# Optimization experiments

Measured on AMD Instinct MI355X. Metric: run time of the kernel, lower is better.

Reference implementation:

```python
import jax, jax.numpy as jnp
import numpy as np

N, K, D, VOCAB = 20000, 32, 128, 100000
NEG = -1e30  # finite large-negative so all-masked rows don't produce NaN softmax


def setup_inputs() -> dict:
    key = jax.random.key(0)
    ks = jax.random.split(key, 10)
    return {
        "nodes": jax.random.randint(ks[0], (N,), 0, VOCAB),
        "neigh_idx": jax.random.randint(ks[1], (N, K), 0, VOCAB),
        "neigh_len": jax.random.randint(ks[2], (N,), 0, K + 1),
        "u2e": jax.random.normal(ks[3], (VOCAB, D), dtype=jnp.float32),
        "W1": jax.random.normal(ks[4], (D, 2 * D), dtype=jnp.float32) * 0.05,
        "b1": jax.random.normal(ks[5], (D,), dtype=jnp.float32) * 0.05,
        "W2": jax.random.normal(ks[6], (D, D), dtype=jnp.float32) * 0.05,
        "b2": jax.random.normal(ks[7], (D,), dtype=jnp.float32) * 0.05,
        "W3": jax.random.normal(ks[8], (1, D), dtype=jnp.float32) * 0.05,
        "b3": jax.random.normal(ks[9], (1,), dtype=jnp.float32) * 0.05,
    }


def reference(nodes, neigh_idx, neigh_len, u2e, W1, b1, W2, b2, W3, b3):
    # self features: [N, D]
    self_feats = u2e[nodes]
    # neighbor features gather: [N, K, D]
    e_u = u2e[neigh_idx]
    # GraphRec Attention: cat(neighbor, self-broadcast) -> MLP -> softmax over K
    x = jnp.concatenate(
        [e_u, jnp.broadcast_to(self_feats[:, None, :], e_u.shape)], axis=-1
    )  # [N, K, 2D]
    h = jax.nn.relu(jnp.einsum("nkf,df->nkd", x, W1) + b1)
    h = jax.nn.relu(jnp.einsum("nkd,ed->nke", h, W2) + b2)
    logits = jnp.einsum("nkd,od->nko", h, W3)[..., 0] + b3[0]  # [N, K]
    mask = jnp.arange(K)[None, :] < neigh_len[:, None]  # [N, K]
    att = jax.nn.softmax(jnp.where(mask, logits, NEG), axis=1)
    att = jnp.where(mask, att, 0.0)  # zero out padded slots (and all-empty rows)
    # attention-weighted neighbor aggregation: [N, D]
    agg = jnp.einsum("nk,nkd->nd", att, e_u)
    has_neigh = (neigh_len > 0)[:, None]
    return jnp.where(has_neigh, (agg + self_feats) * 0.5, self_feats)
```

## Files before the change

### kernel.cpp

```cpp
#include <hip/hip_runtime.h>
#include <hip/hip_bf16.h>
#include <stdint.h>

#define KN 32
#define D  128
#define NNODES 20000
#define GRID 2500
#define ITERS 4
#define VOCAB 100000

#define CONV_BLOCKS 6250
#define PACK_BLOCKS 192
#define SV1_BLOCKS  ((NNODES + 63) / 64)
#define AUX_BLOCKS  (CONV_BLOCKS + PACK_BLOCKS + SV1_BLOCKS)

typedef __bf16 bf16;
typedef __bf16 bf16x8 __attribute__((ext_vector_type(8)));
typedef float  f32x4  __attribute__((ext_vector_type(4)));

#define CHUNK_E 520
#define EU_NODE_E (8 * CHUNK_E)
#define H_STRIDE 136
#define CHUNK_DW 260

#define GL2LDS(src, dst) __builtin_amdgcn_global_load_lds(                 \
    (const __attribute__((address_space(1))) void*)(src),                  \
    (__attribute__((address_space(3))) void*)(dst), 16, 0, 0)

#define MFMA(a, b, c) __builtin_amdgcn_mfma_f32_16x16x32_bf16((a), (b), (c), 0, 0, 0)

__global__ __launch_bounds__(256) void aux_kernel(
    const float* __restrict__ u2e,
    const float* __restrict__ W1,
    const float* __restrict__ W2,
    const int*   __restrict__ nodes,
    bf16*  __restrict__ u2e_bf,
    bf16*  __restrict__ w1p,
    bf16*  __restrict__ w2p,
    float* __restrict__ sv1t)
{
    const int b = blockIdx.x;
    const int t = threadIdx.x;

    if (b < CONV_BLOCKS) {
        size_t i = ((size_t)b * 256 + t) * 8;
        float4 a = *(const float4*)(u2e + i);
        float4 c = *(const float4*)(u2e + i + 4);
        bf16x8 v;
        v[0]=(bf16)a.x; v[1]=(bf16)a.y; v[2]=(bf16)a.z; v[3]=(bf16)a.w;
        v[4]=(bf16)c.x; v[5]=(bf16)c.y; v[6]=(bf16)c.z; v[7]=(bf16)c.w;
        *(bf16x8*)(u2e_bf + i) = v;
        return;
    }
    if (b < CONV_BLOCKS + PACK_BLOCKS) {
        int g = (b - CONV_BLOCKS) * 256 + t;
        if (g < 32768) {
            int j = g & 7, lane = (g >> 3) & 63, kt = (g >> 9) & 7, nt = g >> 12;
            int d = nt * 16 + (lane & 15);
            int f = kt * 32 + ((lane >> 4) << 3) + j;
            w1p[g] = (bf16)W1[d * 256 + f];
        } else if (g < 49152) {
            int u = g - 32768;
            int j = u & 7, lane = (u >> 3) & 63, kt = (u >> 9) & 3, nt = u >> 11;
            int e  = nt * 16 + (lane & 15);
            int dd = kt * 32 + ((lane >> 4) << 3) + j;
            w2p[u] = (bf16)W2[e * 128 + dd];
        }
        return;
    }
    {
        __shared__ alignas(16) float sr[2 * 16 * CHUNK_DW];

        const int sb   = b - CONV_BLOCKS - PACK_BLOCKS;
        const int base = sb * 64;
        const int lane = t & 63;
        const int wave = t >> 6;
        const int ln15 = lane & 15;
        const int quad = lane >> 4;

        {
            const int grp  = wave & 1;
            const int cb   = (wave >> 1) * 8;
            const int half = lane >> 5;
            const int colb = (lane & 31) << 4;
            #pragma unroll
            for (int j = 0; j < 8; ++j) {
                int chunk = cb + j;
                int row = base + grp * 32 + chunk + half * 16;
                int node = nodes[row < NNODES ? row : NNODES - 1];
                GL2LDS((const char*)(u2e + (size_t)node * D) + colb,
                       sr + grp * 16 * CHUNK_DW + chunk * CHUNK_DW);
            }
        }
        __syncthreads();

        const float* g  = sr + (wave & 1) * 16 * CHUNK_DW;
        const int    r0 = ln15 * CHUNK_DW;

        #pragma unroll 1
        for (int np = (wave >> 1) * 2; np <= (wave >> 1) * 2 + 1; ++np) {
            const int nt0 = np * 2;
            bf16x8 b0[4], b1[4];
            #pragma unroll
            for (int kt = 0; kt < 4; ++kt) {
                const float* s0 = W1 + (size_t)(nt0 * 16 + ln15) * 256 + 128 + kt * 32 + quad * 8;
                const float* s1 = W1 + (size_t)((nt0 + 1) * 16 + ln15) * 256 + 128 + kt * 32 + quad * 8;
                f32x4 u0 = *(const f32x4*)(s0), u1 = *(const f32x4*)(s0 + 4);
                f32x4 v0 = *(const f32x4*)(s1), v1 = *(const f32x4*)(s1 + 4);
                bf16x8 bb0, bb1;
                #pragma unroll
                for (int e = 0; e < 4; ++e) {
                    bb0[e] = (bf16)u0[e]; bb0[4 + e] = (bf16)u1[e];
                    bb1[e] = (bf16)v0[e]; bb1[4 + e] = (bf16)v1[e];
                }
                b0[kt] = bb0; b1[kt] = bb1;
            }
            f32x4 c00 = {0.f,0.f,0.f,0.f}, c01 = c00, c10 = c00, c11 = c00;
            #pragma unroll
            for (int kt = 0; kt < 4; ++kt) {
                int off = kt * 32 + quad * 8;
                f32x4 u0 = *(const f32x4*)(g + r0 + off);
                f32x4 u1 = *(const f32x4*)(g + r0 + off + 4);
                f32x4 v0 = *(const f32x4*)(g + r0 + 128 + off);
                f32x4 v1 = *(const f32x4*)(g + r0 + 128 + off + 4);
                bf16x8 a0, a1;
                #pragma unroll
                for (int e = 0; e < 4; ++e) {
                    a0[e] = (bf16)u0[e]; a0[4 + e] = (bf16)u1[e];
                    a1[e] = (bf16)v0[e]; a1[4 + e] = (bf16)v1[e];
                }
                c00 = MFMA(a0, b0[kt], c00);
                c01 = MFMA(a0, b1[kt], c01);
                c10 = MFMA(a1, b0[kt], c10);
                c11 = MFMA(a1, b1[kt], c11);
            }
            #pragma unroll
            for (int r = 0; r < 4; ++r) {
                int row = quad * 4 + r;
                int gr0 = base + (wave & 1) * 32 + row;
                int gr1 = gr0 + 16;
                if (gr0 < NNODES) {
                    sv1t[(size_t)gr0 * D + nt0 * 16 + ln15]       = c00[r];
                    sv1t[(size_t)gr0 * D + (nt0 + 1) * 16 + ln15] = c01[r];
                }
                if (gr1 < NNODES) {
                    sv1t[(size_t)gr1 * D + nt0 * 16 + ln15]       = c10[r];
                    sv1t[(size_t)gr1 * D + (nt0 + 1) * 16 + ln15] = c11[r];
                }
            }
        }
    }
}

__global__ __launch_bounds__(256, 4) void graphrec_agg_kernel(
    const int*   __restrict__ nodes,
    const int*   __restrict__ neigh_idx,
    const int*   __restrict__ neigh_len,
    const float* __restrict__ u2e,
    const bf16*  __restrict__ u2e_bf,
    const float* __restrict__ sv1t,
    const float* __restrict__ b1,
    const float* __restrict__ b2,
    const float* __restrict__ W3,
    const float* __restrict__ b3,
    const bf16*  __restrict__ w1p,
    const bf16*  __restrict__ w2p,
    float*       __restrict__ out)
{
    __shared__ alignas(16) bf16  eu[2 * EU_NODE_E];
    __shared__ alignas(16) float self_f[2 * D];
    __shared__ alignas(16) bf16  h1[2 * KN * H_STRIDE];
    __shared__ float lpart[2][4 * KN];

    const int t    = threadIdx.x;
    const int lane = t & 63;
    const int wave = t >> 6;
    const int ln15 = lane & 15;
    const int quad = lane >> 4;
    const int nt0  = wave * 2;

    const float bias1_0 = b1[nt0 * 16 + ln15];
    const float bias1_1 = b1[(nt0 + 1) * 16 + ln15];
    const float bias2_0 = b2[nt0 * 16 + ln15];
    const float bias2_1 = b2[(nt0 + 1) * 16 + ln15];
    const float w3_0    = W3[nt0 * 16 + ln15];
    const float w3_1    = W3[(nt0 + 1) * 16 + ln15];
    const float b3v     = b3[0];

    bf16x8 w1r[2][4];
    #pragma unroll
    for (int nt = 0; nt < 2; ++nt)
        #pragma unroll
        for (int ft = 0; ft < 4; ++ft)
            w1r[nt][ft] = *(const bf16x8*)(w1p + ((nt0 + nt) * 8 + ft) * 512 + lane * 8);
    bf16x8 w2r[2][4];
    #pragma unroll
    for (int nt = 0; nt < 2; ++nt)
        #pragma unroll
        for (int kt = 0; kt < 4; ++kt)
            w2r[nt][kt] = *(const bf16x8*)(w2p + ((nt0 + nt) * 4 + kt) * 512 + lane * 8);

    #pragma unroll 1
    for (int it = 0; it < ITERS; ++it) {
        const int nA   = blockIdx.x * 8 + it * 2;
        const int lenA = neigh_len[nA];
        const int lenB = neigh_len[nA + 1];

        const float svA0 = sv1t[(size_t)nA * D + nt0 * 16 + ln15];
        const float svA1 = sv1t[(size_t)nA * D + (nt0 + 1) * 16 + ln15];
        const float svB0 = sv1t[(size_t)(nA + 1) * D + nt0 * 16 + ln15];
        const float svB1 = sv1t[(size_t)(nA + 1) * D + (nt0 + 1) * 16 + ln15];

        {
            const int gnd = wave >> 1;
            const int cb  = (wave & 1) * 4;
            #pragma unroll
            for (int j = 0; j < 4; ++j) {
                int chunk = cb + j;
                int idx = neigh_idx[(nA + gnd) * KN + chunk + ((lane >> 4) << 3)];
                GL2LDS(u2e_bf + (size_t)idx * D + ((lane & 15) << 3),
                       eu + gnd * EU_NODE_E + chunk * CHUNK_E);
            }
            if (wave == 0) {
                int sidx = nodes[nA + (lane >> 5)];
                GL2LDS(u2e + (size_t)sidx * D + ((lane & 31) << 2), self_f);
            }
        }
        __syncthreads();

        #pragma unroll 1
        for (int nd = 0; nd < 2; ++nd) {
            const bf16* euN = eu + nd * EU_NODE_E;
            bf16* h1N = h1 + nd * KN * H_STRIDE;

            f32x4 c00 = {0.f,0.f,0.f,0.f}, c01 = c00, c10 = c00, c11 = c00;
            const int rb = (ln15 & 7) * CHUNK_E + (ln15 >> 3) * 128;
            #pragma unroll
            for (int ft = 0; ft < 4; ++ft) {
                bf16x8 a0 = *(const bf16x8*)(euN + rb + ft * 32 + quad * 8);
                bf16x8 a1 = *(const bf16x8*)(euN + rb + 256 + ft * 32 + quad * 8);
                c00 = MFMA(a0, w1r[0][ft], c00);
                c01 = MFMA(a0, w1r[1][ft], c01);
                c10 = MFMA(a1, w1r[0][ft], c10);
                c11 = MFMA(a1, w1r[1][ft], c11);
            }
            const float s0 = nd ? svB0 : svA0;
            const float s1 = nd ? svB1 : svA1;
            #pragma unroll
            for (int r = 0; r < 4; ++r) {
                int row = quad * 4 + r;
                h1N[row * H_STRIDE + nt0 * 16 + ln15]              = (bf16)fmaxf(c00[r] + bias1_0 + s0, 0.f);
                h1N[row * H_STRIDE + (nt0 + 1) * 16 + ln15]        = (bf16)fmaxf(c01[r] + bias1_1 + s1, 0.f);
                h1N[(16 + row) * H_STRIDE + nt0 * 16 + ln15]       = (bf16)fmaxf(c10[r] + bias1_0 + s0, 0.f);
                h1N[(16 + row) * H_STRIDE + (nt0 + 1) * 16 + ln15] = (bf16)fmaxf(c11[r] + bias1_1 + s1, 0.f);
            }
        }
        __syncthreads();

        #pragma unroll 1
        for (int nd = 0; nd < 2; ++nd) {
            const bf16* h1N = h1 + nd * KN * H_STRIDE;
            f32x4 d00 = {0.f,0.f,0.f,0.f}, d01 = d00, d10 = d00, d11 = d00;
            #pragma unroll
            for (int kt = 0; kt < 4; ++kt) {
                bf16x8 a0 = *(const bf16x8*)(h1N + ln15 * H_STRIDE + kt * 32 + quad * 8);
                bf16x8 a1 = *(const bf16x8*)(h1N + (16 + ln15) * H_STRIDE + kt * 32 + quad * 8);
                d00 = MFMA(a0, w2r[0][kt], d00);
                d01 = MFMA(a0, w2r[1][kt], d01);
                d10 = MFMA(a1, w2r[0][kt], d10);
                d11 = MFMA(a1, w2r[1][kt], d11);
            }
            #pragma unroll
            for (int r = 0; r < 4; ++r) {
                float p0 = w3_0 * fmaxf(d00[r] + bias2_0, 0.f)
                         + w3_1 * fmaxf(d01[r] + bias2_1, 0.f);
                float p1 = w3_0 * fmaxf(d10[r] + bias2_0, 0.f)
                         + w3_1 * fmaxf(d11[r] + bias2_1, 0.f);
                #pragma unroll
                for (int o = 1; o < 16; o <<= 1) {
                    p0 += __shfl_xor(p0, o);
                    p1 += __shfl_xor(p1, o);
                }
                if (ln15 == 0) {
                    lpart[nd][wave * KN + quad * 4 + r]      = p0;
                    lpart[nd][wave * KN + 16 + quad * 4 + r] = p1;
                }
            }
        }
        __syncthreads();

        {
            const int nd    = wave >> 1;
            const int dbase = (wave & 1) * 64;
            const int g     = lane >> 3;
            const int l3    = lane & 7;
            const int k     = lane & 31;

            float lg = lpart[nd][k] + lpart[nd][KN + k] + lpart[nd][2 * KN + k]
                     + lpart[nd][3 * KN + k] + b3v;
            const int len = nd ? lenB : lenA;
            bool act = k < len;
            float l = act ? lg : -1e30f;
            float m = l;
            #pragma unroll
            for (int o = 1; o < 32; o <<= 1) m = fmaxf(m, __shfl_xor(m, o));
            float e = act ? expf(l - m) : 0.f;
            float s = e;
            #pragma unroll
            for (int o = 1; o < 32; o <<= 1) s += __shfl_xor(s, o);
            float att = (s > 0.f) ? (e / s) : 0.f;

            const bf16* euN = eu + nd * EU_NODE_E;
            float acc[8] = {0.f,0.f,0.f,0.f,0.f,0.f,0.f,0.f};
            #pragma unroll
            for (int p = 0; p < 4; ++p) {
                int kk = p * 8 + g;
                float attk = __shfl(att, kk);
                bf16x8 v = *(const bf16x8*)(euN + g * CHUNK_E + p * 128 + dbase + l3 * 8);
                #pragma unroll
                for (int j = 0; j < 8; ++j) acc[j] += attk * (float)v[j];
            }
            #pragma unroll
            for (int j = 0; j < 8; ++j) {
                acc[j] += __shfl_xor(acc[j], 8);
                acc[j] += __shfl_xor(acc[j], 16);
                acc[j] += __shfl_xor(acc[j], 32);
            }
            if (g == 0) {
                const float* sfp = self_f + nd * D + dbase + l3 * 8;
                f32x4 sf0 = *(const f32x4*)(sfp);
                f32x4 sf1 = *(const f32x4*)(sfp + 4);
                f32x4 o0, o1;
                #pragma unroll
                for (int j = 0; j < 4; ++j) {
                    o0[j] = (len > 0) ? 0.5f * (acc[j] + sf0[j])     : sf0[j];
                    o1[j] = (len > 0) ? 0.5f * (acc[4 + j] + sf1[j]) : sf1[j];
                }
                float* op = out + (size_t)(nA + nd) * D + dbase + l3 * 8;
                *(f32x4*)(op)     = o0;
                *(f32x4*)(op + 4) = o1;
            }
        }
        __syncthreads();
    }
}

#define FB_EU_NODE_DW (16 * CHUNK_DW)

__global__ __launch_bounds__(256) void pack_weights_kernel(
    const float* __restrict__ W1, const float* __restrict__ W2,
    bf16* __restrict__ w1p, bf16* __restrict__ w2p)
{
    int t = blockIdx.x * 256 + threadIdx.x;
    if (t < 32768) {
        int j = t & 7, lane = (t >> 3) & 63, kt = (t >> 9) & 7, nt = t >> 12;
        int d = nt * 16 + (lane & 15);
        int f = kt * 32 + ((lane >> 4) << 3) + j;
        w1p[t] = (bf16)W1[d * 256 + f];
    } else if (t < 49152) {
        int u = t - 32768;
        int j = u & 7, lane = (u >> 3) & 63, kt = (u >> 9) & 3, nt = u >> 11;
        int e  = nt * 16 + (lane & 15);
        int dd = kt * 32 + ((lane >> 4) << 3) + j;
        w2p[u] = (bf16)W2[e * 128 + dd];
    }
}

__global__ __launch_bounds__(256, 3) void graphrec_agg_fb(
    const int*   __restrict__ nodes,
    const int*   __restrict__ neigh_idx,
    const int*   __restrict__ neigh_len,
    const float* __restrict__ u2e,
    const float* __restrict__ b1,
    const float* __restrict__ b2,
    const float* __restrict__ W3,
    const float* __restrict__ b3,
    const bf16*  __restrict__ w1p,
    const bf16*  __restrict__ w2p,
    float*       __restrict__ out)
{
    __shared__ alignas(16) float eu[2 * FB_EU_NODE_DW];
    __shared__ alignas(16) bf16  h1[2 * KN * H_STRIDE];
    __shared__ alignas(16) float self_f[2 * D];
    __shared__ float lpart[2][4 * KN];
    __shared__ float att_s[2][KN];

    const int t    = threadIdx.x;
    const int lane = t & 63;
    const int wave = t >> 6;
    const int ln15 = lane & 15;
    const int quad = lane >> 4;
    const int nt0  = wave * 2;

    const float bias1_0 = b1[nt0 * 16 + ln15];
    const float bias1_1 = b1[(nt0 + 1) * 16 + ln15];
    const float bias2_0 = b2[nt0 * 16 + ln15];
    const float bias2_1 = b2[(nt0 + 1) * 16 + ln15];
    const float w3_0    = W3[nt0 * 16 + ln15];
    const float w3_1    = W3[(nt0 + 1) * 16 + ln15];
    const float b3v     = b3[0];

    bf16x8 w1r[2][8];
    #pragma unroll
    for (int nt = 0; nt < 2; ++nt)
        #pragma unroll
        for (int ft = 0; ft < 8; ++ft)
            w1r[nt][ft] = *(const bf16x8*)(w1p + ((nt0 + nt) * 8 + ft) * 512 + lane * 8);
    bf16x8 w2r[2][4];
    #pragma unroll
    for (int nt = 0; nt < 2; ++nt)
        #pragma unroll
        for (int kt = 0; kt < 4; ++kt)
            w2r[nt][kt] = *(const bf16x8*)(w2p + ((nt0 + nt) * 4 + kt) * 512 + lane * 8);

    #pragma unroll 1
    for (int it = 0; it < ITERS; ++it) {
        const int nA   = blockIdx.x * 8 + it * 2;
        const int lenA = neigh_len[nA];
        const int lenB = neigh_len[nA + 1];
        {
            const int half = lane >> 5;
            const int colb = (lane & 31) << 4;
            #pragma unroll
            for (int nd = 0; nd < 2; ++nd) {
                #pragma unroll
                for (int j = 0; j < 4; ++j) {
                    int chunk = wave * 4 + j;
                    int idx = neigh_idx[(nA + nd) * KN + chunk + (half << 4)];
                    const char* src = (const char*)(u2e + (size_t)idx * D) + colb;
                    GL2LDS(src, eu + nd * FB_EU_NODE_DW + chunk * CHUNK_DW);
                }
            }
            if (wave == 0) {
                int sidx = nodes[nA + half];
                const char* src = (const char*)(u2e + (size_t)sidx * D) + colb;
                GL2LDS(src, self_f);
            }
        }
        __syncthreads();
        #pragma unroll 1
        for (int nd = 0; nd < 2; ++nd) {
            const float* euN = eu + nd * FB_EU_NODE_DW;
            const float* sfN = self_f + nd * D;
            bf16* h1N = h1 + nd * KN * H_STRIDE;
            f32x4 c00 = {0.f,0.f,0.f,0.f}, c01 = c00, c10 = c00, c11 = c00;
            const int r0 = ln15 * CHUNK_DW;
            #pragma unroll
            for (int ft = 0; ft < 4; ++ft) {
                int off = ft * 32 + quad * 8;
                f32x4 u0 = *(const f32x4*)(euN + r0 + off);
                f32x4 u1 = *(const f32x4*)(euN + r0 + off + 4);
                f32x4 v0 = *(const f32x4*)(euN + r0 + 128 + off);
                f32x4 v1 = *(const f32x4*)(euN + r0 + 128 + off + 4);
                bf16x8 a0, a1;
                #pragma unroll
                for (int e = 0; e < 4; ++e) {
                    a0[e] = (bf16)u0[e]; a0[4 + e] = (bf16)u1[e];
                    a1[e] = (bf16)v0[e]; a1[4 + e] = (bf16)v1[e];
                }
                c00 = MFMA(a0, w1r[0][ft], c00);
                c01 = MFMA(a0, w1r[1][ft], c01);
                c10 = MFMA(a1, w1r[0][ft], c10);
                c11 = MFMA(a1, w1r[1][ft], c11);
            }
            #pragma unroll
            for (int ft = 4; ft < 8; ++ft) {
                int off = (ft - 4) * 32 + quad * 8;
                f32x4 u0 = *(const f32x4*)(sfN + off);
                f32x4 u1 = *(const f32x4*)(sfN + off + 4);
                bf16x8 a;
                #pragma unroll
                for (int e = 0; e < 4; ++e) { a[e] = (bf16)u0[e]; a[4 + e] = (bf16)u1[e]; }
                c00 = MFMA(a, w1r[0][ft], c00);
                c01 = MFMA(a, w1r[1][ft], c01);
                c10 = MFMA(a, w1r[0][ft], c10);
                c11 = MFMA(a, w1r[1][ft], c11);
            }
            #pragma unroll
            for (int r = 0; r < 4; ++r) {
                int row = quad * 4 + r;
                h1N[row * H_STRIDE + nt0 * 16 + ln15]              = (bf16)fmaxf(c00[r] + bias1_0, 0.f);
                h1N[row * H_STRIDE + (nt0 + 1) * 16 + ln15]        = (bf16)fmaxf(c01[r] + bias1_1, 0.f);
                h1N[(16 + row) * H_STRIDE + nt0 * 16 + ln15]       = (bf16)fmaxf(c10[r] + bias1_0, 0.f);
                h1N[(16 + row) * H_STRIDE + (nt0 + 1) * 16 + ln15] = (bf16)fmaxf(c11[r] + bias1_1, 0.f);
            }
        }
        __syncthreads();
        #pragma unroll 1
        for (int nd = 0; nd < 2; ++nd) {
            const bf16* h1N = h1 + nd * KN * H_STRIDE;
            f32x4 d00 = {0.f,0.f,0.f,0.f}, d01 = d00, d10 = d00, d11 = d00;
            #pragma unroll
            for (int kt = 0; kt < 4; ++kt) {
                bf16x8 a0 = *(const bf16x8*)(h1N + ln15 * H_STRIDE + kt * 32 + quad * 8);
                bf16x8 a1 = *(const bf16x8*)(h1N + (16 + ln15) * H_STRIDE + kt * 32 + quad * 8);
                d00 = MFMA(a0, w2r[0][kt], d00);
                d01 = MFMA(a0, w2r[1][kt], d01);
                d10 = MFMA(a1, w2r[0][kt], d10);
                d11 = MFMA(a1, w2r[1][kt], d11);
            }
            #pragma unroll
            for (int r = 0; r < 4; ++r) {
                float p0 = w3_0 * fmaxf(d00[r] + bias2_0, 0.f)
                         + w3_1 * fmaxf(d01[r] + bias2_1, 0.f);
                float p1 = w3_0 * fmaxf(d10[r] + bias2_0, 0.f)
                         + w3_1 * fmaxf(d11[r] + bias2_1, 0.f);
                #pragma unroll
                for (int o = 1; o < 16; o <<= 1) {
                    p0 += __shfl_xor(p0, o);
                    p1 += __shfl_xor(p1, o);
                }
                if (ln15 == 0) {
                    lpart[nd][wave * KN + quad * 4 + r]      = p0;
                    lpart[nd][wave * KN + 16 + quad * 4 + r] = p1;
                }
            }
        }
        __syncthreads();
        if (wave < 2) {
            int nd = wave, k = lane & 31;
            float lg = lpart[nd][k] + lpart[nd][KN + k] + lpart[nd][2 * KN + k]
                     + lpart[nd][3 * KN + k] + b3v;
            int len = nd ? lenB : lenA;
            bool act = (lane < 32) && (k < len);
            float l = act ? lg : -1e30f;
            float m = l;
            #pragma unroll
            for (int o = 1; o < 32; o <<= 1) m = fmaxf(m, __shfl_xor(m, o));
            float e = act ? expf(l - m) : 0.f;
            float s = e;
            #pragma unroll
            for (int o = 1; o < 32; o <<= 1) s += __shfl_xor(s, o);
            if (lane < 32) att_s[nd][k] = (s > 0.f) ? (e / s) : 0.f;
        }
        __syncthreads();
        {
            int nd = t >> 7, d = t & 127;
            const float* euN = eu + nd * FB_EU_NODE_DW;
            float acc = 0.f;
            #pragma unroll
            for (int k = 0; k < KN; ++k)
                acc += att_s[nd][k] * euN[(k & 15) * CHUNK_DW + ((k >> 4) << 7) + d];
            float sf = self_f[nd * D + d];
            int len = nd ? lenB : lenA;
            out[(size_t)(nA + nd) * D + d] = (len > 0) ? 0.5f * (acc + sf) : sf;
        }
        __syncthreads();
    }
}

extern "C" void kernel_launch(void* const* d_in, const int* in_sizes, int n_in,
                              void* d_out, int out_size, void* d_ws, size_t ws_size,
                              hipStream_t stream) {
    const int*   nodes     = (const int*)d_in[0];
    const int*   neigh_idx = (const int*)d_in[1];
    const int*   neigh_len = (const int*)d_in[2];
    const float* u2e       = (const float*)d_in[3];
    const float* W1        = (const float*)d_in[4];
    const float* b1        = (const float*)d_in[5];
    const float* W2        = (const float*)d_in[6];
    const float* b2        = (const float*)d_in[7];
    const float* W3        = (const float*)d_in[8];
    const float* b3        = (const float*)d_in[9];
    float* out = (float*)d_out;

    bf16*  w1p    = (bf16*)d_ws;
    bf16*  w2p    = w1p + 32768;
    bf16*  u2e_bf = (bf16*)((char*)d_ws + 98304);
    float* sv1t   = (float*)((char*)d_ws + 98304 + (size_t)VOCAB * D * 2);
    const size_t need = 98304ull + (size_t)VOCAB * D * 2 + (size_t)NNODES * D * 4;

    if (ws_size >= need) {
        aux_kernel<<<AUX_BLOCKS, 256, 0, stream>>>(u2e, W1, W2, nodes,
                                                   u2e_bf, w1p, w2p, sv1t);
        graphrec_agg_kernel<<<GRID, 256, 0, stream>>>(nodes, neigh_idx, neigh_len,
                                                      u2e, u2e_bf, sv1t, b1, b2,
                                                      W3, b3, w1p, w2p, out);
    } else {
        pack_weights_kernel<<<192, 256, 0, stream>>>(W1, W2, w1p, w2p);
        graphrec_agg_fb<<<GRID, 256, 0, stream>>>(nodes, neigh_idx, neigh_len, u2e,
                                                  b1, b2, W3, b3, w1p, w2p, out);
    }
}
```

Before: 223.1 us.

## Double-buffer neighbor gathers into LDS and simplify per-lane aggregation

Gathered neighbor and self rows now go into two alternating LDS buffers. Each iteration issues the global-to-LDS loads for the next node pair before computing the current one, so the random-access gather overlaps with the MFMA work. Barriers that only guard LDS traffic become a cheaper lgkmcnt wait plus s_barrier. The trailing sync is dropped. The weighted aggregation now has each lane own one feature column and loop over all 32 neighbors with shuffles and scalar LDS reads, replacing the vectorized partial sums and cross-lane reduction. The doubled LDS footprint lowers the occupancy hint from 4 to 3 blocks, and the new aggregation issues many more shuffles and scalar LDS loads.

```diff
diff --git a/kernel.cpp b/kernel.cpp
--- a/kernel.cpp
+++ b/kernel.cpp
@@ -28,6 +28,12 @@
     (__attribute__((address_space(3))) void*)(dst), 16, 0, 0)
 
 #define MFMA(a, b, c) __builtin_amdgcn_mfma_f32_16x16x32_bf16((a), (b), (c), 0, 0, 0)
+
+__device__ __forceinline__ void bar_lds() {
+    asm volatile("s_waitcnt lgkmcnt(0)" ::: "memory");
+    __builtin_amdgcn_s_barrier();
+    asm volatile("" ::: "memory");
+}
 
 __global__ __launch_bounds__(256) void aux_kernel(
     const float* __restrict__ u2e,
@@ -152,7 +158,7 @@
     }
 }
 
-__global__ __launch_bounds__(256, 4) void graphrec_agg_kernel(
+__global__ __launch_bounds__(256, 3) void graphrec_agg_kernel(
     const int*   __restrict__ nodes,
     const int*   __restrict__ neigh_idx,
     const int*   __restrict__ neigh_len,
@@ -167,8 +173,8 @@
     const bf16*  __restrict__ w2p,
     float*       __restrict__ out)
 {
-    __shared__ alignas(16) bf16  eu[2 * EU_NODE_E];
-    __shared__ alignas(16) float self_f[2 * D];
+    __shared__ alignas(16) bf16  eu[2][2 * EU_NODE_E];
+    __shared__ alignas(16) float self_f[2][2 * D];
     __shared__ alignas(16) bf16  h1[2 * KN * H_STRIDE];
     __shared__ float lpart[2][4 * KN];
 
@@ -200,8 +206,27 @@
         for (int kt = 0; kt < 4; ++kt)
             w2r[nt][kt] = *(const bf16x8*)(w2p + ((nt0 + nt) * 4 + kt) * 512 + lane * 8);
 
+    const int gnd = wave >> 1;
+    const int cb  = (wave & 1) * 4;
+
+    {
+        const int nA0 = blockIdx.x * 8;
+        #pragma unroll
+        for (int j = 0; j < 4; ++j) {
+            int chunk = cb + j;
+            int idx = neigh_idx[(nA0 + gnd) * KN + chunk + ((lane >> 4) << 3)];
+            GL2LDS(u2e_bf + (size_t)idx * D + ((lane & 15) << 3),
+                   &eu[0][gnd * EU_NODE_E + chunk * CHUNK_E]);
+        }
+        if (wave == 0) {
+            int sidx = nodes[nA0 + (lane >> 5)];
+            GL2LDS(u2e + (size_t)sidx * D + ((lane & 31) << 2), &self_f[0][0]);
+        }
+    }
+
     #pragma unroll 1
     for (int it = 0; it < ITERS; ++it) {
+        const int buf  = it & 1;
         const int nA   = blockIdx.x * 8 + it * 2;
         const int lenA = neigh_len[nA];
         const int lenB = neigh_len[nA + 1];
@@ -211,26 +236,26 @@
         const float svB0 = sv1t[(size_t)(nA + 1) * D + nt0 * 16 + ln15];
         const float svB1 = sv1t[(size_t)(nA + 1) * D + (nt0 + 1) * 16 + ln15];
 
-        {
-            const int gnd = wave >> 1;
-            const int cb  = (wave & 1) * 4;
+        __syncthreads();
+
+        if (it + 1 < ITERS) {
+            const int nN = nA + 2;
             #pragma unroll
             for (int j = 0; j < 4; ++j) {
                 int chunk = cb + j;
-                int idx = neigh_idx[(nA + gnd) * KN + chunk + ((lane >> 4) << 3)];
+                int idx = neigh_idx[(nN + gnd) * KN + chunk + ((lane >> 4) << 3)];
                 GL2LDS(u2e_bf + (size_t)idx * D + ((lane & 15) << 3),
-                       eu + gnd * EU_NODE_E + chunk * CHUNK_E);
+                       &eu[buf ^ 1][gnd * EU_NODE_E + chunk * CHUNK_E]);
             }
             if (wave == 0) {
-                int sidx = nodes[nA + (lane >> 5)];
-                GL2LDS(u2e + (size_t)sidx * D + ((lane & 31) << 2), self_f);
-            }
-        }
-        __syncthreads();
+                int sidx = nodes[nN + (lane >> 5)];
+                GL2LDS(u2e + (size_t)sidx * D + ((lane & 31) << 2), &self_f[buf ^ 1][0]);
+            }
+        }
 
         #pragma unroll 1
         for (int nd = 0; nd < 2; ++nd) {
-            const bf16* euN = eu + nd * EU_NODE_E;
+            const bf16* euN = &eu[buf][nd * EU_NODE_E];
             bf16* h1N = h1 + nd * KN * H_STRIDE;
 
             f32x4 c00 = {0.f,0.f,0.f,0.f}, c01 = c00, c10 = c00, c11 = c00;
@@ -255,7 +280,7 @@
                 h1N[(16 + row) * H_STRIDE + (nt0 + 1) * 16 + ln15] = (bf16)fmaxf(c11[r] + bias1_1 + s1, 0.f);
             }
         }
-        __syncthreads();
+        bar_lds();
 
         #pragma unroll 1
         for (int nd = 0; nd < 2; ++nd) {
@@ -287,15 +312,11 @@
                 }
             }
         }
-        __syncthreads();
+        bar_lds();
 
         {
-            const int nd    = wave >> 1;
-            const int dbase = (wave & 1) * 64;
-            const int g     = lane >> 3;
-            const int l3    = lane & 7;
-            const int k     = lane & 31;
-
+            const int nd = wave >> 1;
+            const int k  = lane & 31;
             float lg = lpart[nd][k] + lpart[nd][KN + k] + lpart[nd][2 * KN + k]
                      + lpart[nd][3 * KN + k] + b3v;
             const int len = nd ? lenB : lenA;
@@ -310,38 +331,18 @@
             for (int o = 1; o < 32; o <<= 1) s += __shfl_xor(s, o);
             float att = (s > 0.f) ? (e / s) : 0.f;
 
-            const bf16* euN = eu + nd * EU_NODE_E;
-            float acc[8] = {0.f,0.f,0.f,0.f,0.f,0.f,0.f,0.f};
-            #pragma unroll
-            for (int p = 0; p < 4; ++p) {
-                int kk = p * 8 + g;
-                float attk = __shfl(att, kk);
-                bf16x8 v = *(const bf16x8*)(euN + g * CHUNK_E + p * 128 + dbase + l3 * 8);
-                #pragma unroll
-                for (int j = 0; j < 8; ++j) acc[j] += attk * (float)v[j];
-            }
-            #pragma unroll
-            for (int j = 0; j < 8; ++j) {
-                acc[j] += __shfl_xor(acc[j], 8);
-                acc[j] += __shfl_xor(acc[j], 16);
-                acc[j] += __shfl_xor(acc[j], 32);
-            }
-            if (g == 0) {
-                const float* sfp = self_f + nd * D + dbase + l3 * 8;
-                f32x4 sf0 = *(const f32x4*)(sfp);
-                f32x4 sf1 = *(const f32x4*)(sfp + 4);
-                f32x4 o0, o1;
-                #pragma unroll
-                for (int j = 0; j < 4; ++j) {
-                    o0[j] = (len > 0) ? 0.5f * (acc[j] + sf0[j])     : sf0[j];
-                    o1[j] = (len > 0) ? 0.5f * (acc[4 + j] + sf1[j]) : sf1[j];
-                }
-                float* op = out + (size_t)(nA + nd) * D + dbase + l3 * 8;
-                *(f32x4*)(op)     = o0;
-                *(f32x4*)(op + 4) = o1;
-            }
-        }
-        __syncthreads();
+            const int d = (((wave & 1) << 6) + lane) & 127;
+            const bf16* euN = &eu[buf][nd * EU_NODE_E];
+            float acc = 0.f;
+            #pragma unroll
+            for (int k2 = 0; k2 < KN; ++k2) {
+                float a  = __shfl(att, k2);
+                float ev = (float)euN[(k2 & 7) * CHUNK_E + (k2 >> 3) * 128 + d];
+                acc += a * ev;
+            }
+            float sf = self_f[buf][nd * D + d];
+            out[(size_t)(nA + nd) * D + d] = (len > 0) ? 0.5f * (acc + sf) : sf;
+        }
     }
 }
 
```

Result: slower. 229.0 us (+2.6%).

## Use persistent grid-stride loop over node pairs and simplify aggregation

Applied to the files above, without the earlier changes.

Replaces the fixed 2500-block grid, where each block handled 4 iterations of 2 nodes, with a 1024-block persistent grid that strides over 10000 node pairs. This amortizes the per-block weight register loading over more work. It also moves the sv1t loads after the gather issue so they overlap the async LDS loads. The attention-weighted aggregation changes from 8-wide vector loads with cross-lane shuffle reduction to a per-lane scalar loop over all 32 neighbors, which drops the reduction shuffles but issues more scalar LDS reads and att broadcasts.

```diff
diff --git a/kernel.cpp b/kernel.cpp
--- a/kernel.cpp
+++ b/kernel.cpp
@@ -5,8 +5,8 @@
 #define KN 32
 #define D  128
 #define NNODES 20000
-#define GRID 2500
-#define ITERS 4
+#define NPAIRS 10000
+#define GRID 1024
 #define VOCAB 100000
 
 #define CONV_BLOCKS 6250
@@ -200,20 +200,16 @@
         for (int kt = 0; kt < 4; ++kt)
             w2r[nt][kt] = *(const bf16x8*)(w2p + ((nt0 + nt) * 4 + kt) * 512 + lane * 8);
 
+    const int gnd = wave >> 1;
+    const int cb  = (wave & 1) * 4;
+
     #pragma unroll 1
-    for (int it = 0; it < ITERS; ++it) {
-        const int nA   = blockIdx.x * 8 + it * 2;
+    for (int pair = blockIdx.x; pair < NPAIRS; pair += GRID) {
+        const int nA   = pair * 2;
         const int lenA = neigh_len[nA];
         const int lenB = neigh_len[nA + 1];
 
-        const float svA0 = sv1t[(size_t)nA * D + nt0 * 16 + ln15];
-        const float svA1 = sv1t[(size_t)nA * D + (nt0 + 1) * 16 + ln15];
-        const float svB0 = sv1t[(size_t)(nA + 1) * D + nt0 * 16 + ln15];
-        const float svB1 = sv1t[(size_t)(nA + 1) * D + (nt0 + 1) * 16 + ln15];
-
         {
-            const int gnd = wave >> 1;
-            const int cb  = (wave & 1) * 4;
             #pragma unroll
             for (int j = 0; j < 4; ++j) {
                 int chunk = cb + j;
@@ -226,6 +222,12 @@
                 GL2LDS(u2e + (size_t)sidx * D + ((lane & 31) << 2), self_f);
             }
         }
+
+        const float svA0 = sv1t[(size_t)nA * D + nt0 * 16 + ln15];
+        const float svA1 = sv1t[(size_t)nA * D + (nt0 + 1) * 16 + ln15];
+        const float svB0 = sv1t[(size_t)(nA + 1) * D + nt0 * 16 + ln15];
+        const float svB1 = sv1t[(size_t)(nA + 1) * D + (nt0 + 1) * 16 + ln15];
+
         __syncthreads();
 
         #pragma unroll 1
@@ -290,12 +292,8 @@
         __syncthreads();
 
         {
-            const int nd    = wave >> 1;
-            const int dbase = (wave & 1) * 64;
-            const int g     = lane >> 3;
-            const int l3    = lane & 7;
-            const int k     = lane & 31;
-
+            const int nd = wave >> 1;
+            const int k  = lane & 31;
             float lg = lpart[nd][k] + lpart[nd][KN + k] + lpart[nd][2 * KN + k]
                      + lpart[nd][3 * KN + k] + b3v;
             const int len = nd ? lenB : lenA;
@@ -310,36 +308,17 @@
             for (int o = 1; o < 32; o <<= 1) s += __shfl_xor(s, o);
             float att = (s > 0.f) ? (e / s) : 0.f;
 
+            const int d = (((wave & 1) << 6) + lane) & 127;
             const bf16* euN = eu + nd * EU_NODE_E;
-            float acc[8] = {0.f,0.f,0.f,0.f,0.f,0.f,0.f,0.f};
-            #pragma unroll
-            for (int p = 0; p < 4; ++p) {
-                int kk = p * 8 + g;
-                float attk = __shfl(att, kk);
-                bf16x8 v = *(const bf16x8*)(euN + g * CHUNK_E + p * 128 + dbase + l3 * 8);
-                #pragma unroll
-                for (int j = 0; j < 8; ++j) acc[j] += attk * (float)v[j];
-            }
-            #pragma unroll
-            for (int j = 0; j < 8; ++j) {
-                acc[j] += __shfl_xor(acc[j], 8);
-                acc[j] += __shfl_xor(acc[j], 16);
-                acc[j] += __shfl_xor(acc[j], 32);
-            }
-            if (g == 0) {
-                const float* sfp = self_f + nd * D + dbase + l3 * 8;
-                f32x4 sf0 = *(const f32x4*)(sfp);
-                f32x4 sf1 = *(const f32x4*)(sfp + 4);
-                f32x4 o0, o1;
-                #pragma unroll
-                for (int j = 0; j < 4; ++j) {
-                    o0[j] = (len > 0) ? 0.5f * (acc[j] + sf0[j])     : sf0[j];
-                    o1[j] = (len > 0) ? 0.5f * (acc[4 + j] + sf1[j]) : sf1[j];
-                }
-                float* op = out + (size_t)(nA + nd) * D + dbase + l3 * 8;
-                *(f32x4*)(op)     = o0;
-                *(f32x4*)(op + 4) = o1;
-            }
+            float acc = 0.f;
+            #pragma unroll
+            for (int k2 = 0; k2 < KN; ++k2) {
+                float a  = __shfl(att, k2);
+                float ev = (float)euN[(k2 & 7) * CHUNK_E + (k2 >> 3) * 128 + d];
+                acc += a * ev;
+            }
+            float sf = self_f[nd * D + d];
+            out[(size_t)(nA + nd) * D + d] = (len > 0) ? 0.5f * (acc + sf) : sf;
         }
         __syncthreads();
     }
@@ -414,8 +393,8 @@
             w2r[nt][kt] = *(const bf16x8*)(w2p + ((nt0 + nt) * 4 + kt) * 512 + lane * 8);
 
     #pragma unroll 1
-    for (int it = 0; it < ITERS; ++it) {
-        const int nA   = blockIdx.x * 8 + it * 2;
+    for (int pair = blockIdx.x; pair < NPAIRS; pair += GRID) {
+        const int nA   = pair * 2;
         const int lenA = neigh_len[nA];
         const int lenB = neigh_len[nA + 1];
         {
```

Measured after the change: 224.5 us. Within noise of the previous version (+0.6%).
